# Performance work log

Hardware: AMD Instinct MI355X
Metric: run time of the kernel (lower is better)

The kernel has to match this reference:

```python
import jax, jax.numpy as jnp
import numpy as np

T, B, I, H = 512, 64, 1024, 1024
STD = 1.0 / np.sqrt(H)  # reset_parameters: uniform(-std, std) on all params


def setup_inputs() -> dict:
    key = jax.random.key(0)
    ks = jax.random.split(key, 6)
    u = lambda k, shape: jax.random.uniform(k, shape, jnp.float32, -STD, STD)
    return {
        "input_": jax.random.normal(ks[0], (T, B, I), jnp.float32),
        "h0": jnp.zeros((B, H), jnp.float32),
        "c0": jnp.zeros((B, H), jnp.float32),
        "weight_ih": u(ks[1], (4 * H, I)),
        "weight_hh": u(ks[2], (4 * H, H)),
        "bias_ih": u(ks[3], (4 * H,)),
        "bias_hh": u(ks[4], (4 * H,)),
        "retention_ratio": u(ks[5], (H,)),
    }


def reference(input_, h0, c0, weight_ih, weight_hh, bias_ih, bias_hh, retention_ratio):
    # Precompute input-side gate projections for all timesteps: [T, B, 4H]
    x_gates = jnp.einsum('tbi,gi->tbg', input_, weight_ih) + bias_ih + bias_hh
    r = retention_ratio

    def step(carry, xg):
        h, c = carry
        gates = xg + h @ weight_hh.T  # [B, 4H]
        i, f, g, o = jnp.split(gates, 4, axis=1)
        cy = jax.nn.sigmoid(f) * c + jax.nn.sigmoid(i) * jnp.tanh(g)
        hy = jax.nn.sigmoid(o) * jnp.tanh(cy)
        hy = r * h + (1.0 - r) * hy  # low-pass blend
        return (hy, cy), hy

    (hT, cT), outputs = jax.lax.scan(step, (h0, c0), x_gates)
    return outputs, hT, cT
```

## Files before the change

### kernel.cpp

```cpp
#include <hip/hip_runtime.h>
#include <hip/hip_bf16.h>
#include <math.h>

#define T_STEPS 512
#define BATCH   64
#define IN_DIM  1024
#define HID     1024
#define G4      (4 * HID)
#define MTOT    (T_STEPS * BATCH)
#define TBH     ((size_t)T_STEPS * BATCH * HID)

#define BM 128
#define BN 128
#define BK 16
#define LDT 132

__global__ __launch_bounds__(256) void xgemm_kernel(
    const float* __restrict__ A, const float* __restrict__ W,
    const float* __restrict__ bih, const float* __restrict__ bhh,
    float* __restrict__ C) {
  __shared__ float As[BK][LDT];
  __shared__ float Ws[BK][LDT];
  const int tid = threadIdx.x;
  const int m0 = blockIdx.y * BM;
  const int n0 = blockIdx.x * BN;
  const int tx = tid & 15, ty = tid >> 4;
  const int srow = tid >> 2;
  const int scol = (tid & 3) << 2;

  float acc[8][8];
#pragma unroll
  for (int i = 0; i < 8; ++i)
#pragma unroll
    for (int j = 0; j < 8; ++j) acc[i][j] = 0.f;

  const float* Ap0 = A + (size_t)(m0 + srow) * IN_DIM + scol;
  const float* Ap1 = Ap0 + (size_t)64 * IN_DIM;
  const float* Wp0 = W + (size_t)(n0 + srow) * IN_DIM + scol;
  const float* Wp1 = Wp0 + (size_t)64 * IN_DIM;

  for (int k0 = 0; k0 < IN_DIM; k0 += BK) {
    float4 av0 = *(const float4*)(Ap0 + k0);
    float4 av1 = *(const float4*)(Ap1 + k0);
    float4 wv0 = *(const float4*)(Wp0 + k0);
    float4 wv1 = *(const float4*)(Wp1 + k0);
    As[scol + 0][srow]      = av0.x; As[scol + 1][srow]      = av0.y;
    As[scol + 2][srow]      = av0.z; As[scol + 3][srow]      = av0.w;
    As[scol + 0][srow + 64] = av1.x; As[scol + 1][srow + 64] = av1.y;
    As[scol + 2][srow + 64] = av1.z; As[scol + 3][srow + 64] = av1.w;
    Ws[scol + 0][srow]      = wv0.x; Ws[scol + 1][srow]      = wv0.y;
    Ws[scol + 2][srow]      = wv0.z; Ws[scol + 3][srow]      = wv0.w;
    Ws[scol + 0][srow + 64] = wv1.x; Ws[scol + 1][srow + 64] = wv1.y;
    Ws[scol + 2][srow + 64] = wv1.z; Ws[scol + 3][srow + 64] = wv1.w;
    __syncthreads();
#pragma unroll
    for (int k = 0; k < BK; ++k) {
      float4 a0 = *(const float4*)&As[k][ty * 8];
      float4 a1 = *(const float4*)&As[k][ty * 8 + 4];
      float4 w0 = *(const float4*)&Ws[k][tx * 8];
      float4 w1 = *(const float4*)&Ws[k][tx * 8 + 4];
      float a8[8] = {a0.x, a0.y, a0.z, a0.w, a1.x, a1.y, a1.z, a1.w};
      float w8[8] = {w0.x, w0.y, w0.z, w0.w, w1.x, w1.y, w1.z, w1.w};
#pragma unroll
      for (int i = 0; i < 8; ++i)
#pragma unroll
        for (int j = 0; j < 8; ++j)
          acc[i][j] = fmaf(a8[i], w8[j], acc[i][j]);
    }
    __syncthreads();
  }

  float bj[8];
#pragma unroll
  for (int j = 0; j < 8; ++j)
    bj[j] = bih[n0 + tx * 8 + j] + bhh[n0 + tx * 8 + j];
#pragma unroll
  for (int i = 0; i < 8; ++i) {
    float* cp = C + (size_t)(m0 + ty * 8 + i) * G4 + n0 + tx * 8;
    float4 s0 = make_float4(acc[i][0] + bj[0], acc[i][1] + bj[1],
                            acc[i][2] + bj[2], acc[i][3] + bj[3]);
    float4 s1 = make_float4(acc[i][4] + bj[4], acc[i][5] + bj[5],
                            acc[i][6] + bj[6], acc[i][7] + bj[7]);
    *(float4*)cp = s0;
    *(float4*)(cp + 4) = s1;
  }
}

#define NBLK 256
#define BAR_STRIDE 320

__device__ __forceinline__ float sigm(float x) {
  return 1.f / (1.f + __expf(-x));
}
__device__ __forceinline__ float tanh_(float x) {
  return 2.f / (1.f + __expf(-2.f * x)) - 1.f;
}

__device__ __forceinline__ void gridbar(unsigned int* base) {
  __syncthreads();
  if (threadIdx.x == 0) {
    __threadfence();
    unsigned int* leaf = base + (blockIdx.x & 15) * 16;
    unsigned int lv = __hip_atomic_fetch_add(leaf, 1u, __ATOMIC_RELAXED,
                                             __HIP_MEMORY_SCOPE_AGENT);
    if (lv == (NBLK / 16) - 1) {
      unsigned int rv = __hip_atomic_fetch_add(base + 256, 1u, __ATOMIC_RELAXED,
                                               __HIP_MEMORY_SCOPE_AGENT);
      if (rv == 15u)
        __hip_atomic_store(base + 257, 1u, __ATOMIC_RELAXED,
                           __HIP_MEMORY_SCOPE_AGENT);
    }
    while (!__hip_atomic_load(base + 257, __ATOMIC_RELAXED,
                              __HIP_MEMORY_SCOPE_AGENT)) {
      __builtin_amdgcn_s_sleep(2);
    }
    __threadfence();
  }
  __syncthreads();
}

__global__ __launch_bounds__(512) void recur_kernel(
    const float* __restrict__ xg,
    const float* __restrict__ Whh,
    const float* __restrict__ h0, const float* __restrict__ c0,
    const float* __restrict__ ret,
    float* __restrict__ out,
    unsigned int* __restrict__ bar) {
  extern __shared__ float smem[];
  float* Wlds = smem;
  float* part = smem + 32768;

  const int tid = threadIdx.x;
  const int cg = blockIdx.x >> 1;
  const int bh = blockIdx.x & 1;
  const int colbase = cg * 8;
  const int b0 = bh * 32;
  const int lane = tid & 63;
  const int wv = tid >> 6;
  const int khalf = wv & 1;
  const int oct = wv >> 1;
  const int rg = lane & 7;
  const int kc = lane >> 3;

  {
    const int row_loc = tid & 31;
    const int kq = tid >> 5;
    const int gate = row_loc >> 3, colz = row_loc & 7;
    const int rgw = row_loc >> 2, rr = row_loc & 3;
    const float* wrow = Whh + (size_t)(gate * HID + colbase + colz) * HID;
    for (int k4 = 0; k4 < 64; k4 += 4) {
      const int k = kq * 64 + k4;
      float4 w = *(const float4*)(wrow + k);
      float vals[4] = {w.x, w.y, w.z, w.w};
      const int q = k >> 2;
      const int base = (k >> 9) * 65536 + ((((q >> 3) & 15) * 4) << 10) +
                       ((q & 7) << 7) + (rgw << 4) + (rr << 2);
#pragma unroll
      for (int e = 0; e < 4; ++e)
        *(float*)((char*)Wlds + base + (e << 10)) = vals[e];
    }
  }

  const int ucol = tid & 7;
  const int ubl = tid >> 3;
  float c_reg = 0.f, h_reg = 0.f, r_coef = 0.f;
  if (tid < 256) {
    int gb = b0 + ubl, gc = colbase + ucol;
    c_reg = c0[gb * HID + gc];
    h_reg = h0[gb * HID + gc];
    r_coef = ret[gc];
  }

  const char* wbase = (const char*)Wlds + khalf * 65536 + lane * 16;
  const int qbase = khalf * 128 + kc;

  __syncthreads();

  for (int t = 0; t < T_STEPS; ++t) {
    const float* hsrc =
        (t == 0) ? h0 : (out + (size_t)(t - 1) * BATCH * HID);
    const float4* hq = (const float4*)(hsrc + (size_t)(b0 + oct * 8) * HID);

    float xgv[4];
    if (tid < 256) {
      const float* xp =
          xg + ((size_t)t * BATCH + b0 + ubl) * G4 + colbase + ucol;
#pragma unroll
      for (int q = 0; q < 4; ++q) xgv[q] = xp[q * HID];
    }

    const char* wb = wbase;
    asm volatile("" : "+v"(wb));

    float acc[4][8];
#pragma unroll
    for (int r = 0; r < 4; ++r)
#pragma unroll
      for (int b = 0; b < 8; ++b) acc[r][b] = 0.f;

#pragma unroll 4
    for (int j = 0; j < 16; ++j) {
      float4 ha[8];
#pragma unroll
      for (int b = 0; b < 8; ++b)
        ha[b] = hq[(size_t)b * 256 + qbase + 8 * j];
#pragma unroll
      for (int e = 0; e < 4; ++e) {
        float wa[4];
        *(float4*)wa = *(const float4*)(wb + ((j * 4 + e) << 10));
#pragma unroll
        for (int r = 0; r < 4; ++r)
#pragma unroll
          for (int b = 0; b < 8; ++b)
            acc[r][b] = fmaf(wa[r], ((const float*)&ha[b])[e], acc[r][b]);
      }
    }

#pragma unroll
    for (int r = 0; r < 4; ++r)
#pragma unroll
      for (int b = 0; b < 8; ++b) {
        float v = acc[r][b];
        v += __shfl_xor(v, 8, 64);
        v += __shfl_xor(v, 16, 64);
        v += __shfl_xor(v, 32, 64);
        acc[r][b] = v;
      }
    if (lane < 8) {
#pragma unroll
      for (int r = 0; r < 4; ++r)
#pragma unroll
        for (int b = 0; b < 8; ++b)
          part[(khalf * 32 + lane * 4 + r) * 33 + oct * 8 + b] = acc[r][b];
    }
    __syncthreads();

    if (tid < 256) {
      float g[4];
#pragma unroll
      for (int q = 0; q < 4; ++q) {
        int row = q * 8 + ucol;
        g[q] = part[row * 33 + ubl] + part[(32 + row) * 33 + ubl] + xgv[q];
      }
      float ig = sigm(g[0]);
      float fg = sigm(g[1]);
      float gg = tanh_(g[2]);
      float og = sigm(g[3]);
      float cy = fg * c_reg + ig * gg;
      float hy = og * tanh_(cy);
      hy = r_coef * h_reg + (1.f - r_coef) * hy;
      c_reg = cy;
      h_reg = hy;
      size_t oidx = ((size_t)t * BATCH + b0 + ubl) * HID + colbase + ucol;
      out[oidx] = hy;
      if (t == T_STEPS - 1) {
        size_t tb = TBH + (size_t)(b0 + ubl) * HID + colbase + ucol;
        out[tb] = hy;
        out[tb + (size_t)BATCH * HID] = cy;
      }
    }

    if (t + 1 < T_STEPS) {
      gridbar(bar + (size_t)t * BAR_STRIDE);
    }
  }
}

extern "C" void kernel_launch(void* const* d_in, const int* in_sizes, int n_in,
                              void* d_out, int out_size, void* d_ws,
                              size_t ws_size, hipStream_t stream) {
  const float* input = (const float*)d_in[0];
  const float* h0    = (const float*)d_in[1];
  const float* c0    = (const float*)d_in[2];
  const float* wih   = (const float*)d_in[3];
  const float* whh   = (const float*)d_in[4];
  const float* bih   = (const float*)d_in[5];
  const float* bhh   = (const float*)d_in[6];
  const float* ret   = (const float*)d_in[7];
  float* out = (float*)d_out;

  unsigned int* bar = (unsigned int*)d_ws;
  float* xg = (float*)((char*)d_ws + (1 << 20));

  hipMemsetAsync(d_ws, 0, (size_t)T_STEPS * BAR_STRIDE * 4, stream);

  dim3 g1(G4 / BN, MTOT / BM);
  xgemm_kernel<<<g1, 256, 0, stream>>>(input, wih, bih, bhh, xg);

  const size_t recur_lds = (32768 + 2 * 32 * 33) * sizeof(float);
  recur_kernel<<<NBLK, 512, recur_lds, stream>>>(xg, whh, h0, c0, ret, out,
                                                 bar);
}
```

Before: 18.18 ms.

## Spread grid barrier release flags and double-buffer hidden-state loads

The grid barrier's single release flag becomes 16 flags, one per group of 16 blocks, each on its own cache line. The aim is to reduce contention while all blocks poll, at the cost of 16 stores by the last arriver. The recurrent matvec loop now double-buffers the h loads across k-chunks so global loads overlap the FMAs, which raises register pressure. The barrier region stride and the workspace offset grow to fit the new flag layout.

```diff
diff --git a/kernel.cpp b/kernel.cpp
--- a/kernel.cpp
+++ b/kernel.cpp
@@ -87,7 +87,7 @@
 }
 
 #define NBLK 256
-#define BAR_STRIDE 320
+#define BAR_STRIDE 800
 
 __device__ __forceinline__ float sigm(float x) {
   return 1.f / (1.f + __expf(-x));
@@ -96,21 +96,25 @@
   return 2.f / (1.f + __expf(-2.f * x)) - 1.f;
 }
 
-__device__ __forceinline__ void gridbar(unsigned int* base) {
+__device__ __forceinline__ void gridbar(unsigned int* base, int bid) {
   __syncthreads();
   if (threadIdx.x == 0) {
     __threadfence();
-    unsigned int* leaf = base + (blockIdx.x & 15) * 16;
+    unsigned int* leaf = base + (bid & 15) * 16;
     unsigned int lv = __hip_atomic_fetch_add(leaf, 1u, __ATOMIC_RELAXED,
                                              __HIP_MEMORY_SCOPE_AGENT);
     if (lv == (NBLK / 16) - 1) {
       unsigned int rv = __hip_atomic_fetch_add(base + 256, 1u, __ATOMIC_RELAXED,
                                                __HIP_MEMORY_SCOPE_AGENT);
-      if (rv == 15u)
-        __hip_atomic_store(base + 257, 1u, __ATOMIC_RELAXED,
-                           __HIP_MEMORY_SCOPE_AGENT);
-    }
-    while (!__hip_atomic_load(base + 257, __ATOMIC_RELAXED,
+      if (rv == 15u) {
+#pragma unroll
+        for (int g2 = 0; g2 < 16; ++g2)
+          __hip_atomic_store(base + 260 + g2 * 32, 1u, __ATOMIC_RELAXED,
+                             __HIP_MEMORY_SCOPE_AGENT);
+      }
+    }
+    unsigned int* myflag = base + 260 + (bid >> 4) * 32;
+    while (!__hip_atomic_load(myflag, __ATOMIC_RELAXED,
                               __HIP_MEMORY_SCOPE_AGENT)) {
       __builtin_amdgcn_s_sleep(2);
     }
@@ -139,8 +143,6 @@
   const int wv = tid >> 6;
   const int khalf = wv & 1;
   const int oct = wv >> 1;
-  const int rg = lane & 7;
-  const int kc = lane >> 3;
 
   {
     const int row_loc = tid & 31;
@@ -172,14 +174,16 @@
   }
 
   const char* wbase = (const char*)Wlds + khalf * 65536 + lane * 16;
-  const int qbase = khalf * 128 + kc;
+  const int qbase = khalf * 128 + (lane >> 3);
+  const int bid = blockIdx.x;
 
   __syncthreads();
 
   for (int t = 0; t < T_STEPS; ++t) {
     const float* hsrc =
         (t == 0) ? h0 : (out + (size_t)(t - 1) * BATCH * HID);
-    const float4* hq = (const float4*)(hsrc + (size_t)(b0 + oct * 8) * HID);
+    const float4* hqt =
+        (const float4*)(hsrc + (size_t)(b0 + oct * 8) * HID) + qbase;
 
     float xgv[4];
     if (tid < 256) {
@@ -198,21 +202,38 @@
 #pragma unroll
       for (int b = 0; b < 8; ++b) acc[r][b] = 0.f;
 
-#pragma unroll 4
-    for (int j = 0; j < 16; ++j) {
-      float4 ha[8];
-#pragma unroll
-      for (int b = 0; b < 8; ++b)
-        ha[b] = hq[(size_t)b * 256 + qbase + 8 * j];
+    float4 haA[8], haB[8];
+#pragma unroll
+    for (int b = 0; b < 8; ++b) haA[b] = hqt[b * 256];
+
+#pragma unroll
+    for (int jj = 0; jj < 8; ++jj) {
+      const int j0 = 2 * jj, j1 = 2 * jj + 1;
+#pragma unroll
+      for (int b = 0; b < 8; ++b) haB[b] = hqt[b * 256 + 8 * j1];
 #pragma unroll
       for (int e = 0; e < 4; ++e) {
         float wa[4];
-        *(float4*)wa = *(const float4*)(wb + ((j * 4 + e) << 10));
+        *(float4*)wa = *(const float4*)(wb + ((j0 * 4 + e) << 10));
 #pragma unroll
         for (int r = 0; r < 4; ++r)
 #pragma unroll
           for (int b = 0; b < 8; ++b)
-            acc[r][b] = fmaf(wa[r], ((const float*)&ha[b])[e], acc[r][b]);
+            acc[r][b] = fmaf(wa[r], ((const float*)&haA[b])[e], acc[r][b]);
+      }
+      if (jj < 7) {
+#pragma unroll
+        for (int b = 0; b < 8; ++b) haA[b] = hqt[b * 256 + 8 * (j1 + 1)];
+      }
+#pragma unroll
+      for (int e = 0; e < 4; ++e) {
+        float wa[4];
+        *(float4*)wa = *(const float4*)(wb + ((j1 * 4 + e) << 10));
+#pragma unroll
+        for (int r = 0; r < 4; ++r)
+#pragma unroll
+          for (int b = 0; b < 8; ++b)
+            acc[r][b] = fmaf(wa[r], ((const float*)&haB[b])[e], acc[r][b]);
       }
     }
 
@@ -261,7 +282,7 @@
     }
 
     if (t + 1 < T_STEPS) {
-      gridbar(bar + (size_t)t * BAR_STRIDE);
+      gridbar(bar + (size_t)t * BAR_STRIDE, bid);
     }
   }
 }
@@ -280,7 +301,7 @@
   float* out = (float*)d_out;
 
   unsigned int* bar = (unsigned int*)d_ws;
-  float* xg = (float*)((char*)d_ws + (1 << 20));
+  float* xg = (float*)((char*)d_ws + (2 << 20));
 
   hipMemsetAsync(d_ws, 0, (size_t)T_STEPS * BAR_STRIDE * 4, stream);
 
```

Measured after the change: 16.69 ms. -8.2%, faster.
